# Optimization experiments

Hardware: AMD Instinct MI355X
Metric: run time of the kernel (lower is better)

The kernel has to match this reference:

```python
import jax, jax.numpy as jnp
import numpy as np

N_NODES = 50000
N_EDGES = 640000
HIDDEN = 128
LN_EPS = 1e-5


def setup_inputs() -> dict:
    key = jax.random.key(0)
    k_h, k_e, k_w1, k_w2 = jax.random.split(key, 4)
    s = 1.0 / np.sqrt(HIDDEN)
    return {
        "h": jax.random.normal(k_h, (N_NODES, HIDDEN), dtype=jnp.float32),
        "edge_index": jax.random.randint(k_e, (2, N_EDGES), 0, N_NODES, dtype=jnp.int32),
        "W1": jax.random.normal(k_w1, (HIDDEN, HIDDEN), dtype=jnp.float32) * s,
        "b1": jnp.zeros((HIDDEN,), dtype=jnp.float32),
        "W2": jax.random.normal(k_w2, (HIDDEN, HIDDEN), dtype=jnp.float32) * s,
        "b2": jnp.zeros((HIDDEN,), dtype=jnp.float32),
        "eps": jnp.zeros((), dtype=jnp.float32),  # GINConv train_eps init
        "gamma": jnp.ones((HIDDEN,), dtype=jnp.float32),
        "beta": jnp.zeros((HIDDEN,), dtype=jnp.float32),
    }


def reference(h, edge_index, W1, b1, W2, b2, eps, gamma, beta):
    src, dst = edge_index[0], edge_index[1]
    # GIN aggregation: sum of neighbor features scattered to destination nodes
    agg = jax.ops.segment_sum(h[src], dst, num_segments=h.shape[0])  # (N, D)
    z = (1.0 + eps) * h + agg
    # 2-layer MLP: Linear -> ReLU -> Linear (torch Linear: x @ W.T + b)
    z = jax.nn.relu(z @ W1.T + b1)
    h_conv = z @ W2.T + b2
    # residual + LayerNorm + ReLU (dropout is identity in eval mode)
    h_res = h_conv + h
    mu = jnp.mean(h_res, axis=-1, keepdims=True)
    var = jnp.var(h_res, axis=-1, keepdims=True)
    h_norm = (h_res - mu) * jax.lax.rsqrt(var + LN_EPS) * gamma + beta
    return jax.nn.relu(h_norm)
```

## Files before the change

kernel.cpp:

```cpp
#include <hip/hip_runtime.h>

#define HID 128
#define LN_EPS 1e-5f

typedef __attribute__((ext_vector_type(8))) short bf16x8;
typedef __attribute__((ext_vector_type(4))) float f32x4;

static __device__ __forceinline__ unsigned short f2bf(float f) {
  unsigned int x = __float_as_uint(f);
  x += 0x7fffu + ((x >> 16) & 1u);
  return (unsigned short)(x >> 16);
}
static __device__ __forceinline__ float bflo(unsigned int u) { return __uint_as_float(u << 16); }
static __device__ __forceinline__ float bfhi(unsigned int u) { return __uint_as_float(u & 0xffff0000u); }

__global__ __launch_bounds__(256) void k_count(const int* __restrict__ ei,
                                               int* __restrict__ counts, int nE) {
  const int e = blockIdx.x * 256 + threadIdx.x;
  if (e >= nE) return;
  atomicAdd(&counts[ei[nE + e]], 1);
}

__global__ __launch_bounds__(256) void k_scan1(const int* __restrict__ counts,
                                               int* __restrict__ offsets,
                                               int* __restrict__ bsum, int n) {
  __shared__ int sm[256];
  const int t = threadIdx.x;
  const int i = blockIdx.x * 256 + t;
  const int v = (i < n) ? counts[i] : 0;
  int incl = v;
  sm[t] = incl;
  __syncthreads();
#pragma unroll
  for (int off = 1; off < 256; off <<= 1) {
    const int other = (t >= off) ? sm[t - off] : 0;
    __syncthreads();
    incl += other;
    sm[t] = incl;
    __syncthreads();
  }
  if (i < n) offsets[i] = incl - v;
  if (t == 255) bsum[blockIdx.x] = incl;
}

__global__ __launch_bounds__(256) void k_scan2(const int* __restrict__ bsum,
                                               int* __restrict__ ebase,
                                               int* __restrict__ offsets,
                                               int nb, int n) {
  __shared__ int sm[256];
  const int t = threadIdx.x;
  const int v = (t < nb) ? bsum[t] : 0;
  int incl = v;
  sm[t] = incl;
  __syncthreads();
#pragma unroll
  for (int off = 1; off < 256; off <<= 1) {
    const int other = (t >= off) ? sm[t - off] : 0;
    __syncthreads();
    incl += other;
    sm[t] = incl;
    __syncthreads();
  }
  if (t < nb) ebase[t] = incl - v;
  if (t == 255) offsets[n] = incl;
}

__global__ __launch_bounds__(256) void k_scan3(int* __restrict__ offsets,
                                               int* __restrict__ cursors,
                                               const int* __restrict__ ebase, int n) {
  const int i = blockIdx.x * 256 + threadIdx.x;
  if (i >= n) return;
  const int o = offsets[i] + ebase[blockIdx.x];
  offsets[i] = o;
  cursors[i] = o;
}

__global__ __launch_bounds__(256) void k_bucket(const int* __restrict__ ei,
                                                int* __restrict__ cursors,
                                                int* __restrict__ esrc, int nE) {
  const int e = blockIdx.x * 256 + threadIdx.x;
  if (e >= nE) return;
  const int s = ei[e];
  const int d = ei[nE + e];
  const int pos = atomicAdd(&cursors[d], 1);
  esrc[pos] = s;
}

__global__ __launch_bounds__(256) void k_tobf(const float* __restrict__ in,
                                              unsigned int* __restrict__ out, int n4) {
  const int stride = gridDim.x * 256;
  for (int i = blockIdx.x * 256 + threadIdx.x; i < n4; i += stride) {
    const float4 v = reinterpret_cast<const float4*>(in)[i];
    uint2 p;
    p.x = (unsigned)f2bf(v.x) | ((unsigned)f2bf(v.y) << 16);
    p.y = (unsigned)f2bf(v.z) | ((unsigned)f2bf(v.w) << 16);
    reinterpret_cast<uint2*>(out)[i] = p;
  }
}

__global__ __launch_bounds__(256) void k_gather(const unsigned short* __restrict__ hbf,
                                                const int* __restrict__ offsets,
                                                const int* __restrict__ esrc,
                                                const float* __restrict__ eps,
                                                unsigned short* __restrict__ zbf, int nNodes) {
  const int gid = blockIdx.x * 256 + threadIdx.x;
  const int node = gid >> 5;
  if (node >= nNodes) return;
  const int col4 = (threadIdx.x & 31) * 4;
  const float c = 1.0f + eps[0];

  const uint2 hv = *reinterpret_cast<const uint2*>(hbf + (size_t)node * HID + col4);
  float a0 = c * bflo(hv.x), a1 = c * bfhi(hv.x);
  float a2 = c * bflo(hv.y), a3 = c * bfhi(hv.y);

  const int beg = offsets[node], end = offsets[node + 1];
  int e = beg;
  for (; e + 1 < end; e += 2) {
    const int s0 = esrc[e], s1 = esrc[e + 1];
    const uint2 v0 = *reinterpret_cast<const uint2*>(hbf + (size_t)s0 * HID + col4);
    const uint2 v1 = *reinterpret_cast<const uint2*>(hbf + (size_t)s1 * HID + col4);
    a0 += bflo(v0.x) + bflo(v1.x);
    a1 += bfhi(v0.x) + bfhi(v1.x);
    a2 += bflo(v0.y) + bflo(v1.y);
    a3 += bfhi(v0.y) + bfhi(v1.y);
  }
  if (e < end) {
    const uint2 v0 = *reinterpret_cast<const uint2*>(hbf + (size_t)esrc[e] * HID + col4);
    a0 += bflo(v0.x); a1 += bfhi(v0.x); a2 += bflo(v0.y); a3 += bfhi(v0.y);
  }
  uint2 o;
  o.x = (unsigned)f2bf(a0) | ((unsigned)f2bf(a1) << 16);
  o.y = (unsigned)f2bf(a2) | ((unsigned)f2bf(a3) << 16);
  *reinterpret_cast<uint2*>(zbf + (size_t)node * HID + col4) = o;
}

__global__ __launch_bounds__(256) void k_mm1(unsigned short* zy,
                                             const unsigned short* __restrict__ wbf,
                                             const float* __restrict__ bias, int nTiles) {
  const int wave = threadIdx.x >> 6;
  const int l = threadIdx.x & 63;
  const int mtile = blockIdx.x * 4 + wave;
  if (mtile >= nTiles) return;
  const int row0 = mtile * 16;
  const int lr = l & 15;
  const int lq = l >> 4;

  bf16x8 a[4];
#pragma unroll
  for (int ks = 0; ks < 4; ++ks)
    a[ks] = *reinterpret_cast<const bf16x8*>(zy + (size_t)(row0 + lr) * HID + ks * 32 + lq * 8);

  f32x4 acc[8];
#pragma unroll
  for (int nt = 0; nt < 8; ++nt) acc[nt] = (f32x4){0.f, 0.f, 0.f, 0.f};

#pragma unroll
  for (int nt = 0; nt < 8; ++nt) {
    const unsigned short* wb = wbf + (size_t)(nt * 16 + lr) * HID + lq * 8;
#pragma unroll
    for (int ks = 0; ks < 4; ++ks) {
      const bf16x8 b = *reinterpret_cast<const bf16x8*>(wb + ks * 32);
      acc[nt] = __builtin_amdgcn_mfma_f32_16x16x32_bf16(a[ks], b, acc[nt], 0, 0, 0);
    }
  }

#pragma unroll
  for (int nt = 0; nt < 8; ++nt) {
    const int c = nt * 16 + lr;
    const float bs = bias[c];
#pragma unroll
    for (int r = 0; r < 4; ++r) {
      const int row = row0 + lq * 4 + r;
      zy[(size_t)row * HID + c] = f2bf(fmaxf(acc[nt][r] + bs, 0.f));
    }
  }
}

__global__ __launch_bounds__(256) void k_mm2(const unsigned short* __restrict__ y1,
                                             const unsigned short* __restrict__ wbf,
                                             const float* __restrict__ bias,
                                             const float* __restrict__ h,
                                             const float* __restrict__ gamma,
                                             const float* __restrict__ beta,
                                             float* __restrict__ out, int nTiles) {
  const int wave = threadIdx.x >> 6;
  const int l = threadIdx.x & 63;
  const int mtile = blockIdx.x * 4 + wave;
  if (mtile >= nTiles) return;
  const int row0 = mtile * 16;
  const int lr = l & 15;
  const int lq = l >> 4;

  bf16x8 a[4];
#pragma unroll
  for (int ks = 0; ks < 4; ++ks)
    a[ks] = *reinterpret_cast<const bf16x8*>(y1 + (size_t)(row0 + lr) * HID + ks * 32 + lq * 8);

  f32x4 acc[8];
#pragma unroll
  for (int nt = 0; nt < 8; ++nt) acc[nt] = (f32x4){0.f, 0.f, 0.f, 0.f};

#pragma unroll
  for (int nt = 0; nt < 8; ++nt) {
    const unsigned short* wb = wbf + (size_t)(nt * 16 + lr) * HID + lq * 8;
#pragma unroll
    for (int ks = 0; ks < 4; ++ks) {
      const bf16x8 b = *reinterpret_cast<const bf16x8*>(wb + ks * 32);
      acc[nt] = __builtin_amdgcn_mfma_f32_16x16x32_bf16(a[ks], b, acc[nt], 0, 0, 0);
    }
  }

#pragma unroll
  for (int nt = 0; nt < 8; ++nt) {
    const int c = nt * 16 + lr;
    const float bs = bias[c];
#pragma unroll
    for (int r = 0; r < 4; ++r) {
      const int row = row0 + lq * 4 + r;
      acc[nt][r] += bs + h[(size_t)row * HID + c];
    }
  }

  float mu_[4], rstd_[4];
#pragma unroll
  for (int r = 0; r < 4; ++r) {
    float s = 0.f, ss = 0.f;
#pragma unroll
    for (int nt = 0; nt < 8; ++nt) { const float v = acc[nt][r]; s += v; ss += v * v; }
#pragma unroll
    for (int m = 1; m < 16; m <<= 1) {
      s += __shfl_xor(s, m, 64);
      ss += __shfl_xor(ss, m, 64);
    }
    const float mu = s * (1.f / 128.f);
    const float var = ss * (1.f / 128.f) - mu * mu;
    mu_[r] = mu;
    rstd_[r] = rsqrtf(var + LN_EPS);
  }

#pragma unroll
  for (int nt = 0; nt < 8; ++nt) {
    const int c = nt * 16 + lr;
    const float g = gamma[c], be = beta[c];
#pragma unroll
    for (int r = 0; r < 4; ++r) {
      const int row = row0 + lq * 4 + r;
      const float o = (acc[nt][r] - mu_[r]) * rstd_[r] * g + be;
      out[(size_t)row * HID + c] = fmaxf(o, 0.f);
    }
  }
}

extern "C" void kernel_launch(void* const* d_in, const int* in_sizes, int n_in,
                              void* d_out, int out_size, void* d_ws, size_t ws_size,
                              hipStream_t stream) {
  const float* h     = (const float*)d_in[0];
  const int*   ei    = (const int*)d_in[1];
  const float* W1    = (const float*)d_in[2];
  const float* b1    = (const float*)d_in[3];
  const float* W2    = (const float*)d_in[4];
  const float* b2    = (const float*)d_in[5];
  const float* eps   = (const float*)d_in[6];
  const float* gamma = (const float*)d_in[7];
  const float* beta  = (const float*)d_in[8];

  const int nNodes = in_sizes[0] / HID;
  const int nE     = in_sizes[1] / 2;
  const int nb     = (nNodes + 255) / 256;

  int* counts  = (int*)d_ws;
  int* offsets = counts + nNodes;
  int* cursors = offsets + nNodes + 1;
  int* bsum    = cursors + nNodes;
  int* ebase   = bsum + nb;
  int* esrc    = counts + 150400;
  unsigned short* hbf  = (unsigned short*)(esrc + nE);
  unsigned short* zbf  = hbf + (size_t)nNodes * HID;
  unsigned short* w1bf = zbf + (size_t)nNodes * HID;
  unsigned short* w2bf = w1bf + HID * HID;

  hipMemsetAsync(counts, 0, (size_t)nNodes * sizeof(int), stream);

  const int eblocks = (nE + 255) / 256;
  k_count<<<eblocks, 256, 0, stream>>>(ei, counts, nE);
  k_scan1<<<nb, 256, 0, stream>>>(counts, offsets, bsum, nNodes);
  k_scan2<<<1, 256, 0, stream>>>(bsum, ebase, offsets, nb, nNodes);
  k_scan3<<<nb, 256, 0, stream>>>(offsets, cursors, ebase, nNodes);
  k_bucket<<<eblocks, 256, 0, stream>>>(ei, cursors, esrc, nE);

  k_tobf<<<2048, 256, 0, stream>>>(h,  (unsigned int*)hbf,  nNodes * HID / 4);
  k_tobf<<<16,   256, 0, stream>>>(W1, (unsigned int*)w1bf, HID * HID / 4);
  k_tobf<<<16,   256, 0, stream>>>(W2, (unsigned int*)w2bf, HID * HID / 4);

  k_gather<<<(nNodes * 32 + 255) / 256, 256, 0, stream>>>(hbf, offsets, esrc, eps, zbf, nNodes);

  const int nTiles = nNodes / 16;
  const int mblocks = (nTiles + 3) / 4;
  k_mm1<<<mblocks, 256, 0, stream>>>(zbf, w1bf, b1, nTiles);
  k_mm2<<<mblocks, 256, 0, stream>>>(zbf, w2bf, b2, h, gamma, beta, (float*)d_out, nTiles);
}
```

Baseline: 244.2 us.

## Fuse gather, both MLP matmuls and LayerNorm into one LDS-tiled kernel

```diff
diff --git a/kernel.cpp b/kernel.cpp
--- a/kernel.cpp
+++ b/kernel.cpp
@@ -2,6 +2,7 @@
 
 #define HID 128
 #define LN_EPS 1e-5f
+#define LDSW 136
 
 typedef __attribute__((ext_vector_type(8))) short bf16x8;
 typedef __attribute__((ext_vector_type(4))) float f32x4;
@@ -86,77 +87,97 @@
   esrc[pos] = s;
 }
 
-__global__ __launch_bounds__(256) void k_tobf(const float* __restrict__ in,
-                                              unsigned int* __restrict__ out, int n4) {
+__global__ __launch_bounds__(256) void k_tobf3(const float* __restrict__ h,
+                                               const float* __restrict__ w1,
+                                               const float* __restrict__ w2,
+                                               uint2* __restrict__ hb,
+                                               uint2* __restrict__ w1b,
+                                               uint2* __restrict__ w2b,
+                                               int nh4, int nw4) {
+  const int total = nh4 + 2 * nw4;
   const int stride = gridDim.x * 256;
-  for (int i = blockIdx.x * 256 + threadIdx.x; i < n4; i += stride) {
-    const float4 v = reinterpret_cast<const float4*>(in)[i];
+  for (int i = blockIdx.x * 256 + threadIdx.x; i < total; i += stride) {
+    const float* src;
+    uint2* dst;
+    int off;
+    if (i < nh4) { src = h; dst = hb; off = i; }
+    else if (i < nh4 + nw4) { src = w1; dst = w1b; off = i - nh4; }
+    else { src = w2; dst = w2b; off = i - nh4 - nw4; }
+    const float4 v = reinterpret_cast<const float4*>(src)[off];
     uint2 p;
     p.x = (unsigned)f2bf(v.x) | ((unsigned)f2bf(v.y) << 16);
     p.y = (unsigned)f2bf(v.z) | ((unsigned)f2bf(v.w) << 16);
-    reinterpret_cast<uint2*>(out)[i] = p;
-  }
-}
-
-__global__ __launch_bounds__(256) void k_gather(const unsigned short* __restrict__ hbf,
-                                                const int* __restrict__ offsets,
-                                                const int* __restrict__ esrc,
-                                                const float* __restrict__ eps,
-                                                unsigned short* __restrict__ zbf, int nNodes) {
-  const int gid = blockIdx.x * 256 + threadIdx.x;
-  const int node = gid >> 5;
-  if (node >= nNodes) return;
-  const int col4 = (threadIdx.x & 31) * 4;
+    dst[off] = p;
+  }
+}
+
+__global__ __launch_bounds__(256) void k_fused(const unsigned short* __restrict__ hbf,
+                                               const int* __restrict__ offsets,
+                                               const int* __restrict__ esrc,
+                                               const float* __restrict__ eps,
+                                               const unsigned short* __restrict__ w1,
+                                               const unsigned short* __restrict__ w2,
+                                               const float* __restrict__ b1,
+                                               const float* __restrict__ b2,
+                                               const float* __restrict__ h,
+                                               const float* __restrict__ gamma,
+                                               const float* __restrict__ beta,
+                                               float* __restrict__ out, int nNodes) {
+  __shared__ unsigned short zt[64][LDSW];
+  const int t = threadIdx.x;
+  const int tile64 = blockIdx.x * 64;
   const float c = 1.0f + eps[0];
 
-  const uint2 hv = *reinterpret_cast<const uint2*>(hbf + (size_t)node * HID + col4);
-  float a0 = c * bflo(hv.x), a1 = c * bfhi(hv.x);
-  float a2 = c * bflo(hv.y), a3 = c * bfhi(hv.y);
-
-  const int beg = offsets[node], end = offsets[node + 1];
-  int e = beg;
-  for (; e + 1 < end; e += 2) {
-    const int s0 = esrc[e], s1 = esrc[e + 1];
-    const uint2 v0 = *reinterpret_cast<const uint2*>(hbf + (size_t)s0 * HID + col4);
-    const uint2 v1 = *reinterpret_cast<const uint2*>(hbf + (size_t)s1 * HID + col4);
-    a0 += bflo(v0.x) + bflo(v1.x);
-    a1 += bfhi(v0.x) + bfhi(v1.x);
-    a2 += bflo(v0.y) + bflo(v1.y);
-    a3 += bfhi(v0.y) + bfhi(v1.y);
-  }
-  if (e < end) {
-    const uint2 v0 = *reinterpret_cast<const uint2*>(hbf + (size_t)esrc[e] * HID + col4);
-    a0 += bflo(v0.x); a1 += bfhi(v0.x); a2 += bflo(v0.y); a3 += bfhi(v0.y);
-  }
-  uint2 o;
-  o.x = (unsigned)f2bf(a0) | ((unsigned)f2bf(a1) << 16);
-  o.y = (unsigned)f2bf(a2) | ((unsigned)f2bf(a3) << 16);
-  *reinterpret_cast<uint2*>(zbf + (size_t)node * HID + col4) = o;
-}
-
-__global__ __launch_bounds__(256) void k_mm1(unsigned short* zy,
-                                             const unsigned short* __restrict__ wbf,
-                                             const float* __restrict__ bias, int nTiles) {
-  const int wave = threadIdx.x >> 6;
-  const int l = threadIdx.x & 63;
-  const int mtile = blockIdx.x * 4 + wave;
-  if (mtile >= nTiles) return;
-  const int row0 = mtile * 16;
+#pragma unroll
+  for (int p = 0; p < 8; ++p) {
+    const int r = p * 8 + (t >> 5);
+    const int node = tile64 + r;
+    const int col4 = (t & 31) * 4;
+    if (node < nNodes) {
+      const uint2 hv = *reinterpret_cast<const uint2*>(hbf + (size_t)node * HID + col4);
+      float a0 = c * bflo(hv.x), a1 = c * bfhi(hv.x);
+      float a2 = c * bflo(hv.y), a3 = c * bfhi(hv.y);
+      const int beg = offsets[node], end = offsets[node + 1];
+      int e = beg;
+      for (; e + 1 < end; e += 2) {
+        const int s0 = esrc[e], s1 = esrc[e + 1];
+        const uint2 v0 = *reinterpret_cast<const uint2*>(hbf + (size_t)s0 * HID + col4);
+        const uint2 v1 = *reinterpret_cast<const uint2*>(hbf + (size_t)s1 * HID + col4);
+        a0 += bflo(v0.x) + bflo(v1.x);
+        a1 += bfhi(v0.x) + bfhi(v1.x);
+        a2 += bflo(v0.y) + bflo(v1.y);
+        a3 += bfhi(v0.y) + bfhi(v1.y);
+      }
+      if (e < end) {
+        const uint2 v0 = *reinterpret_cast<const uint2*>(hbf + (size_t)esrc[e] * HID + col4);
+        a0 += bflo(v0.x); a1 += bfhi(v0.x); a2 += bflo(v0.y); a3 += bfhi(v0.y);
+      }
+      uint2 o;
+      o.x = (unsigned)f2bf(a0) | ((unsigned)f2bf(a1) << 16);
+      o.y = (unsigned)f2bf(a2) | ((unsigned)f2bf(a3) << 16);
+      *reinterpret_cast<uint2*>(&zt[r][col4]) = o;
+    }
+  }
+  __syncthreads();
+
+  const int l = t & 63;
   const int lr = l & 15;
   const int lq = l >> 4;
+  const int row0w = (t >> 6) * 16;
+  const int grow0 = tile64 + row0w;
+  if (grow0 >= nNodes) return;
 
   bf16x8 a[4];
 #pragma unroll
   for (int ks = 0; ks < 4; ++ks)
-    a[ks] = *reinterpret_cast<const bf16x8*>(zy + (size_t)(row0 + lr) * HID + ks * 32 + lq * 8);
+    a[ks] = *reinterpret_cast<const bf16x8*>(&zt[row0w + lr][ks * 32 + lq * 8]);
 
   f32x4 acc[8];
 #pragma unroll
   for (int nt = 0; nt < 8; ++nt) acc[nt] = (f32x4){0.f, 0.f, 0.f, 0.f};
-
-#pragma unroll
-  for (int nt = 0; nt < 8; ++nt) {
-    const unsigned short* wb = wbf + (size_t)(nt * 16 + lr) * HID + lq * 8;
+#pragma unroll
+  for (int nt = 0; nt < 8; ++nt) {
+    const unsigned short* wb = w1 + (size_t)(nt * 16 + lr) * HID + lq * 8;
 #pragma unroll
     for (int ks = 0; ks < 4; ++ks) {
       const bf16x8 b = *reinterpret_cast<const bf16x8*>(wb + ks * 32);
@@ -166,58 +187,38 @@
 
 #pragma unroll
   for (int nt = 0; nt < 8; ++nt) {
-    const int c = nt * 16 + lr;
-    const float bs = bias[c];
-#pragma unroll
-    for (int r = 0; r < 4; ++r) {
-      const int row = row0 + lq * 4 + r;
-      zy[(size_t)row * HID + c] = f2bf(fmaxf(acc[nt][r] + bs, 0.f));
-    }
-  }
-}
-
-__global__ __launch_bounds__(256) void k_mm2(const unsigned short* __restrict__ y1,
-                                             const unsigned short* __restrict__ wbf,
-                                             const float* __restrict__ bias,
-                                             const float* __restrict__ h,
-                                             const float* __restrict__ gamma,
-                                             const float* __restrict__ beta,
-                                             float* __restrict__ out, int nTiles) {
-  const int wave = threadIdx.x >> 6;
-  const int l = threadIdx.x & 63;
-  const int mtile = blockIdx.x * 4 + wave;
-  if (mtile >= nTiles) return;
-  const int row0 = mtile * 16;
-  const int lr = l & 15;
-  const int lq = l >> 4;
-
-  bf16x8 a[4];
+    const int cc = nt * 16 + lr;
+    const float bs = b1[cc];
+#pragma unroll
+    for (int r = 0; r < 4; ++r)
+      zt[row0w + lq * 4 + r][cc] = f2bf(fmaxf(acc[nt][r] + bs, 0.f));
+  }
+
+  bf16x8 a2[4];
 #pragma unroll
   for (int ks = 0; ks < 4; ++ks)
-    a[ks] = *reinterpret_cast<const bf16x8*>(y1 + (size_t)(row0 + lr) * HID + ks * 32 + lq * 8);
-
-  f32x4 acc[8];
+    a2[ks] = *reinterpret_cast<const bf16x8*>(&zt[row0w + lr][ks * 32 + lq * 8]);
+
 #pragma unroll
   for (int nt = 0; nt < 8; ++nt) acc[nt] = (f32x4){0.f, 0.f, 0.f, 0.f};
-
-#pragma unroll
-  for (int nt = 0; nt < 8; ++nt) {
-    const unsigned short* wb = wbf + (size_t)(nt * 16 + lr) * HID + lq * 8;
+#pragma unroll
+  for (int nt = 0; nt < 8; ++nt) {
+    const unsigned short* wb = w2 + (size_t)(nt * 16 + lr) * HID + lq * 8;
 #pragma unroll
     for (int ks = 0; ks < 4; ++ks) {
       const bf16x8 b = *reinterpret_cast<const bf16x8*>(wb + ks * 32);
-      acc[nt] = __builtin_amdgcn_mfma_f32_16x16x32_bf16(a[ks], b, acc[nt], 0, 0, 0);
-    }
-  }
-
-#pragma unroll
-  for (int nt = 0; nt < 8; ++nt) {
-    const int c = nt * 16 + lr;
-    const float bs = bias[c];
+      acc[nt] = __builtin_amdgcn_mfma_f32_16x16x32_bf16(a2[ks], b, acc[nt], 0, 0, 0);
+    }
+  }
+
+#pragma unroll
+  for (int nt = 0; nt < 8; ++nt) {
+    const int cc = nt * 16 + lr;
+    const float bs = b2[cc];
 #pragma unroll
     for (int r = 0; r < 4; ++r) {
-      const int row = row0 + lq * 4 + r;
-      acc[nt][r] += bs + h[(size_t)row * HID + c];
+      const int row = grow0 + lq * 4 + r;
+      acc[nt][r] += bs + h[(size_t)row * HID + cc];
     }
   }
 
@@ -237,16 +238,15 @@
     mu_[r] = mu;
     rstd_[r] = rsqrtf(var + LN_EPS);
   }
-
-#pragma unroll
-  for (int nt = 0; nt < 8; ++nt) {
-    const int c = nt * 16 + lr;
-    const float g = gamma[c], be = beta[c];
+#pragma unroll
+  for (int nt = 0; nt < 8; ++nt) {
+    const int cc = nt * 16 + lr;
+    const float g = gamma[cc], be = beta[cc];
 #pragma unroll
     for (int r = 0; r < 4; ++r) {
-      const int row = row0 + lq * 4 + r;
+      const int row = grow0 + lq * 4 + r;
       const float o = (acc[nt][r] - mu_[r]) * rstd_[r] * g + be;
-      out[(size_t)row * HID + c] = fmaxf(o, 0.f);
+      out[(size_t)row * HID + cc] = fmaxf(o, 0.f);
     }
   }
 }
@@ -275,27 +275,21 @@
   int* ebase   = bsum + nb;
   int* esrc    = counts + 150400;
   unsigned short* hbf  = (unsigned short*)(esrc + nE);
-  unsigned short* zbf  = hbf + (size_t)nNodes * HID;
-  unsigned short* w1bf = zbf + (size_t)nNodes * HID;
+  unsigned short* w1bf = hbf + (size_t)nNodes * HID;
   unsigned short* w2bf = w1bf + HID * HID;
 
   hipMemsetAsync(counts, 0, (size_t)nNodes * sizeof(int), stream);
 
   const int eblocks = (nE + 255) / 256;
+  k_tobf3<<<2048, 256, 0, stream>>>(h, W1, W2, (uint2*)hbf, (uint2*)w1bf, (uint2*)w2bf,
+                                    nNodes * HID / 4, HID * HID / 4);
   k_count<<<eblocks, 256, 0, stream>>>(ei, counts, nE);
   k_scan1<<<nb, 256, 0, stream>>>(counts, offsets, bsum, nNodes);
   k_scan2<<<1, 256, 0, stream>>>(bsum, ebase, offsets, nb, nNodes);
   k_scan3<<<nb, 256, 0, stream>>>(offsets, cursors, ebase, nNodes);
   k_bucket<<<eblocks, 256, 0, stream>>>(ei, cursors, esrc, nE);
 
-  k_tobf<<<2048, 256, 0, stream>>>(h,  (unsigned int*)hbf,  nNodes * HID / 4);
-  k_tobf<<<16,   256, 0, stream>>>(W1, (unsigned int*)w1bf, HID * HID / 4);
-  k_tobf<<<16,   256, 0, stream>>>(W2, (unsigned int*)w2bf, HID * HID / 4);
-
-  k_gather<<<(nNodes * 32 + 255) / 256, 256, 0, stream>>>(hbf, offsets, esrc, eps, zbf, nNodes);
-
-  const int nTiles = nNodes / 16;
-  const int mblocks = (nTiles + 3) / 4;
-  k_mm1<<<mblocks, 256, 0, stream>>>(zbf, w1bf, b1, nTiles);
-  k_mm2<<<mblocks, 256, 0, stream>>>(zbf, w2bf, b2, h, gamma, beta, (float*)d_out, nTiles);
-}
+  const int fblocks = (nNodes + 63) / 64;
+  k_fused<<<fblocks, 256, 0, stream>>>(hbf, offsets, esrc, eps, w1bf, w2bf,
+                                       b1, b2, h, gamma, beta, (float*)d_out, nNodes);
+}
```

New measurement: 258.7 us. 1.06x slower.
